# Kernel optimization log

Hardware: AMD Instinct MI355X
Metric: run time of the kernel (lower is better)

The kernel has to match this reference:

```python
import jax, jax.numpy as jnp
import numpy as np

B, T, D, K, NF = 4, 1024, 1024, 4, 4
MAXD = 256          # TemporalEncoding max_delta
NC = 32             # ConceptGraph n_concepts
LN_EPS = 1e-5


def setup_inputs() -> dict:
    key = jax.random.key(0)
    ks = jax.random.split(key, 12)
    s = 0.02  # weight init scale
    return {
        "x": jax.random.normal(ks[0], (B, T, D), jnp.float32),
        "routed_tokens": jax.random.normal(ks[1], (B, T, K, D), jnp.float32),
        "sim": jax.random.normal(ks[2], (B, T, K), jnp.float32),
        # per-function logic Linear(3D->D), LayerNorm(D), gate Linear(3D->D)
        "Wl": jax.random.normal(ks[3], (NF, 3 * D, D), jnp.float32) * s,
        "bl": jnp.zeros((NF, D), jnp.float32),
        "ln_g": jnp.ones((NF, D), jnp.float32),
        "ln_b": jnp.zeros((NF, D), jnp.float32),
        "Wg": jax.random.normal(ks[4], (NF, 3 * D, D), jnp.float32) * s,
        "bg": jnp.zeros((NF, D), jnp.float32),
        # fn_selector Linear(D -> NF)
        "Wsel": jax.random.normal(ks[5], (D, NF), jnp.float32) * s,
        "bsel": jnp.zeros((NF,), jnp.float32),
        # temporal embedding table [2*max_delta+1, D]
        "delta_table": jax.random.normal(ks[6], (2 * MAXD + 1, D), jnp.float32) * s,
        # VQ codebook (ConceptGraph.embedding buffer)
        "codebook": jax.random.normal(ks[7], (NC, D), jnp.float32),
        "topk_indices": jax.random.randint(ks[8], (B, T, K), 0, T),
    }


def reference(x, routed_tokens, sim, Wl, bl, ln_g, ln_b, Wg, bg,
              Wsel, bsel, delta_table, codebook, topk_indices):
    Bx, Tx, Dx = x.shape
    Kx = routed_tokens.shape[2]
    N = Bx * Tx

    # temporal encoding: delta = t - topk_index, clamped into table range
    t = jnp.arange(Tx)[None, :, None]
    idx = jnp.clip(t - topk_indices + MAXD, 0, 2 * MAXD)
    de = delta_table[idx].reshape(N, Kx, Dx)            # [N,K,D]

    xf = x.reshape(N, Dx)
    rf = routed_tokens.reshape(N, Kx, Dx)
    sf = sim.reshape(N, Kx)

    tok = jnp.broadcast_to(xf[:, None, :], (N, Kx, Dx))
    comb = jnp.concatenate([tok, rf, de], axis=-1)       # [N,K,3D]

    # all NF reasoning functions at once: logic MLP + GELU + LayerNorm
    h = jnp.einsum('nkc,fcd->fnkd', comb, Wl) + bl[:, None, None, :]
    h = jax.nn.gelu(h, approximate=False)
    mu = jnp.mean(h, axis=-1, keepdims=True)
    var = jnp.var(h, axis=-1, keepdims=True)
    h = (h - mu) / jnp.sqrt(var + LN_EPS)
    h = h * ln_g[:, None, None, :] + ln_b[:, None, None, :]  # [F,N,K,D]

    sw = jax.nn.softmax(sf, axis=-1)                     # [N,K]
    arg = jnp.einsum('nk,fnkd->fnd', sw, h)              # [F,N,D]

    tok_f = jnp.broadcast_to(xf[None], (Wl.shape[0], N, Dx))
    gin = jnp.concatenate([tok_f, arg, arg], axis=-1)    # [F,N,3D]
    gate = jax.nn.sigmoid(jnp.einsum('fnc,fcd->fnd', gin, Wg) + bg[:, None, :])

    fw = jax.nn.softmax(xf @ Wsel + bsel, axis=-1)       # [N,F]
    proposed = jnp.einsum('nf,fnd->nd', fw, arg)
    gsum = jnp.einsum('nf,fnd->nd', fw, gate)
    uf = proposed * gsum                                 # [N,D] updated tokens

    # ConceptGraph VQ (eval: no EMA update): pairwise dist, argmin, gather
    d2 = (jnp.sum(uf * uf, axis=1, keepdims=True)
          - 2.0 * uf @ codebook.T
          + jnp.sum(codebook * codebook, axis=1))        # [N,NC]
    enc = jnp.argmin(d2, axis=1)                         # [N]
    quant = codebook[enc]                                # [N,D]
    out = uf + jax.lax.stop_gradient(quant - uf)         # straight-through
    return out.reshape(Bx, Tx, Dx)
```

## Files before the change

### kernel.cpp

```cpp
#include <hip/hip_runtime.h>
#include <hip/hip_bf16.h>
#include <cmath>


typedef __bf16 bf16x8 __attribute__((ext_vector_type(8)));
typedef float  f32x4  __attribute__((ext_vector_type(4)));

__device__ __forceinline__ float gelu_f(float v) {
    return 0.5f * v * (1.0f + erff(v * 0.7071067811865476f));
}

__device__ __forceinline__ void split8(const float* v, bf16x8& H, bf16x8& L) {
#pragma unroll
    for (int j = 0; j < 8; ++j) {
        float x = v[j];
        __bf16 h = (__bf16)x;
        H[j] = h;
        L[j] = (__bf16)(x - (float)h);
    }
}

#define GLL16(src, dst)                                                        \
    __builtin_amdgcn_global_load_lds(                                          \
        (const __attribute__((address_space(1))) void*)(src),                  \
        (__attribute__((address_space(3))) void*)(dst), 16, 0, 0)

#define SWZ_DECODE()                                                           \
    int bx, by, bz;                                                            \
    {                                                                          \
        const int nx = gridDim.x, ny = gridDim.y;                              \
        const int nwg = nx * ny * (int)gridDim.z;                              \
        const int bid = blockIdx.x + nx * (blockIdx.y + ny * blockIdx.z);      \
        const int q = nwg >> 3;                                                \
        const int rm = (bid & 7) * q + (bid >> 3);                             \
        bx = rm % nx; by = (rm / nx) % ny; bz = rm / (nx * ny);                \
    }

__global__ __launch_bounds__(256) void precvt_img(
    const float* __restrict__ W, char* __restrict__ img,
    int krowBase, int nktLog, int sumFromKt)
{
    const int u = blockIdx.x * 256 + threadIdx.x;
    const int col = u & 127;
    const int kt  = (u >> 7) & ((1 << nktLog) - 1);
    const int ct  = (u >> (7 + nktLog)) & 7;
    const int f   = u >> (10 + nktLog);
    const int colg = ct * 128 + col;
    const float* Wf = W + (size_t)f * 3072 * 1024;
    const bool sum2 = (kt >= sumFromKt);

    float vv[32];
#pragma unroll
    for (int j = 0; j < 32; ++j) {
        int k = krowBase + kt * 32 + j;
        float v = Wf[(size_t)k * 1024 + colg];
        if (sum2) v += Wf[(size_t)(k + 1024) * 1024 + colg];
        vv[j] = v;
    }
    char* tb = img + ((((size_t)f * 8 + ct) << nktLog) + kt) * 16384;
    const int swz = (col >> 1) & 3;
#pragma unroll
    for (int g = 0; g < 4; ++g) {
        bf16x8 H, L; split8(&vv[g * 8], H, L);
        char* dst = tb + col * 64 + ((g ^ swz) << 4);
        *(bf16x8*)dst = H;
        *(bf16x8*)(dst + 8192) = L;
    }
}

#define WRITEA_SPLIT(AB)                                                       \
    {                                                                          \
        int row = tid >> 2, ag = tid & 3;                                      \
        bf16x8 H, L; split8(ra[0], H, L);                                      \
        char* d = (AB) + row * 64 + ((ag ^ ((row >> 1) & 3)) << 4);            \
        *(bf16x8*)d = H; *(bf16x8*)(d + 8192) = L;                             \
        int row2 = row + 64;                                                   \
        split8(ra[1], H, L);                                                   \
        char* d2 = (AB) + row2 * 64 + ((ag ^ ((row2 >> 1) & 3)) << 4);         \
        *(bf16x8*)d2 = H; *(bf16x8*)(d2 + 8192) = L;                           \
    }

#define LOADB_IMG(KT, BB)                                                      \
    {                                                                          \
        const char* sb = Bt + (size_t)(KT) * 16384 + boff;                     \
        char* db = (BB) + boff;                                                \
        GLL16(sb,        db);                                                  \
        GLL16(sb + 1024, db + 1024);                                           \
        GLL16(sb + 2048, db + 2048);                                           \
        GLL16(sb + 3072, db + 3072);                                           \
    }

#define MFMA32(AB, BB)                                                         \
    {                                                                          \
        bf16x8 ah[4], al[4], bh[4], bl_[4];                                    \
        _Pragma("unroll")                                                      \
        for (int mi = 0; mi < 4; ++mi) {                                       \
            const char* pa = (AB) + (wr + mi * 16 + rl) * 64 + goff;           \
            ah[mi] = *(const bf16x8*)pa;                                       \
            al[mi] = *(const bf16x8*)(pa + 8192);                              \
        }                                                                      \
        _Pragma("unroll")                                                      \
        for (int ni = 0; ni < 4; ++ni) {                                       \
            const char* pb = (BB) + (wc + ni * 16 + rl) * 64 + goff;           \
            bh[ni]  = *(const bf16x8*)pb;                                      \
            bl_[ni] = *(const bf16x8*)(pb + 8192);                             \
        }                                                                      \
        _Pragma("unroll")                                                      \
        for (int mi = 0; mi < 4; ++mi)                                         \
            _Pragma("unroll")                                                  \
            for (int ni = 0; ni < 4; ++ni) {                                   \
                acc[mi][ni] = __builtin_amdgcn_mfma_f32_16x16x32_bf16(ah[mi], bh[ni],  acc[mi][ni], 0, 0, 0); \
                acc[mi][ni] = __builtin_amdgcn_mfma_f32_16x16x32_bf16(ah[mi], bl_[ni], acc[mi][ni], 0, 0, 0); \
                acc[mi][ni] = __builtin_amdgcn_mfma_f32_16x16x32_bf16(al[mi], bh[ni],  acc[mi][ni], 0, 0, 0); \
            }                                                                  \
    }

__global__ __launch_bounds__(256, 2) void gemm_img(
    const float* __restrict__ A, int rowBase,
    const char* __restrict__ img, int fimgBase,
    float* __restrict__ C, size_t cStrideZ)
{
    __shared__ __align__(16) char lds[65536];
    const int tid = threadIdx.x, wid = tid >> 6, lane = tid & 63;
    SWZ_DECODE();
    const int bm0 = bx * 128, bn0 = by * 128;
    const int fimg = fimgBase + bz;
    const char* Bt = img + (size_t)((fimg * 8 + by) << 5) * 16384;
    float* Cp = C + (size_t)bz * cStrideZ;
    const int wr = (wid >> 1) * 64, wc = (wid & 1) * 64;
    const int g = lane >> 4, rl = lane & 15;
    const int goff = ((g ^ ((rl >> 1) & 3)) << 4);
    const int boff = wid * 4096 + lane * 16;
    char* A0 = lds;            char* A1 = lds + 16384;
    char* B0 = lds + 32768;    char* B1 = lds + 49152;

    const float* abase = A + (size_t)(rowBase + bm0 + (tid >> 2)) * 1024 + (tid & 3) * 8;
    float ra[2][8];
#define LOADA_H(KT)                                                            \
    {                                                                          \
        const float* s = abase + (KT) * 32;                                    \
        *(float4*)&ra[0][0] = ((const float4*)s)[0];                           \
        *(float4*)&ra[0][4] = ((const float4*)s)[1];                           \
        const float* s2 = s + 64 * 1024;                                       \
        *(float4*)&ra[1][0] = ((const float4*)s2)[0];                          \
        *(float4*)&ra[1][4] = ((const float4*)s2)[1];                          \
    }

    f32x4 acc[4][4];
    f32x4 zero = {0.f, 0.f, 0.f, 0.f};
#pragma unroll
    for (int i = 0; i < 4; ++i)
#pragma unroll
        for (int j = 0; j < 4; ++j) acc[i][j] = zero;

    LOADA_H(0)
    LOADB_IMG(0, B0)
    WRITEA_SPLIT(A0)
    LOADA_H(1)
    __syncthreads();
    for (int kt = 0; kt < 32; ++kt) {
        char* Ac = (kt & 1) ? A1 : A0;  char* Bc = (kt & 1) ? B1 : B0;
        char* An = (kt & 1) ? A0 : A1;  char* Bn = (kt & 1) ? B0 : B1;
        if (kt < 31) {
            LOADB_IMG(kt + 1, Bn)
            WRITEA_SPLIT(An)
            if (kt < 30) LOADA_H(kt + 2)
        }
        MFMA32(Ac, Bc)
        __syncthreads();
    }
#undef LOADA_H

    const int cg = lane & 15, rg = (lane >> 4) * 4;
#pragma unroll
    for (int mi = 0; mi < 4; ++mi)
#pragma unroll
        for (int i = 0; i < 4; ++i) {
            int row_out = bm0 + wr + mi * 16 + rg + i;
#pragma unroll
            for (int ni = 0; ni < 4; ++ni) {
                int col = bn0 + wc + ni * 16 + cg;
                Cp[(size_t)row_out * 1024 + col] = acc[mi][ni][i];
            }
        }
}

__global__ __launch_bounds__(256, 2) void gate_img(
    const float* __restrict__ x, const float* __restrict__ arg,
    const char* __restrict__ img, const float* __restrict__ fw,
    const float* __restrict__ bg, float* __restrict__ g2, int fbase)
{
    __shared__ __align__(16) char lds[65536];
    const int tid = threadIdx.x, wid = tid >> 6, lane = tid & 63;
    SWZ_DECODE();
    const int bm0 = bx * 128, bn0 = by * 128;
    const int z = bz, f = fbase + z;
    const float* argf = arg + (size_t)f * 4096 * 1024;
    const char* Bt = img + (size_t)((f * 8 + by) << 6) * 16384;
    const int wr = (wid >> 1) * 64, wc = (wid & 1) * 64;
    const int g = lane >> 4, rl = lane & 15;
    const int goff = ((g ^ ((rl >> 1) & 3)) << 4);
    const int boff = wid * 4096 + lane * 16;
    char* A0 = lds;            char* A1 = lds + 16384;
    char* B0 = lds + 32768;    char* B1 = lds + 49152;

    const int arow = bm0 + (tid >> 2);
    const int akc  = (tid & 3) * 8;
    float ra[2][8];
#define LOADA_G(KT)                                                            \
    {                                                                          \
        int k0 = (KT) * 32 + akc;                                              \
        const float* base = (k0 < 1024) ? x : (argf - 1024);                   \
        const float* s  = base + (size_t)arow * 1024 + k0;                     \
        const float* s2 = base + (size_t)(arow + 64) * 1024 + k0;              \
        *(float4*)&ra[0][0] = ((const float4*)s)[0];                           \
        *(float4*)&ra[0][4] = ((const float4*)s)[1];                           \
        *(float4*)&ra[1][0] = ((const float4*)s2)[0];                          \
        *(float4*)&ra[1][4] = ((const float4*)s2)[1];                          \
    }

    f32x4 acc[4][4];
    f32x4 zero = {0.f, 0.f, 0.f, 0.f};
#pragma unroll
    for (int i = 0; i < 4; ++i)
#pragma unroll
        for (int j = 0; j < 4; ++j) acc[i][j] = zero;

    LOADA_G(0)
    LOADB_IMG(0, B0)
    WRITEA_SPLIT(A0)
    LOADA_G(1)
    __syncthreads();
    for (int kt = 0; kt < 64; ++kt) {
        char* Ac = (kt & 1) ? A1 : A0;  char* Bc = (kt & 1) ? B1 : B0;
        char* An = (kt & 1) ? A0 : A1;  char* Bn = (kt & 1) ? B0 : B1;
        if (kt < 63) {
            LOADB_IMG(kt + 1, Bn)
            WRITEA_SPLIT(An)
            if (kt < 62) LOADA_G(kt + 2)
        }
        MFMA32(Ac, Bc)
        __syncthreads();
    }
#undef LOADA_G

    const int cg = lane & 15, rg = (lane >> 4) * 4;
    const bool accum = (fbase > 0);
#pragma unroll
    for (int mi = 0; mi < 4; ++mi)
#pragma unroll
        for (int i = 0; i < 4; ++i) {
            int row_out = bm0 + wr + mi * 16 + rg + i;
            float fwv = fw[(size_t)row_out * 4 + f];
#pragma unroll
            for (int ni = 0; ni < 4; ++ni) {
                int col = bn0 + wc + ni * 16 + cg;
                float v = acc[mi][ni][i] + bg[f * 1024 + col];
                float s = fwv / (1.0f + expf(-v));
                size_t off = ((size_t)z * 4096 + row_out) * 1024 + col;
                if (accum) g2[off] += s; else g2[off] = s;
            }
        }
}

#define STAGE_WRITE64()                                                        \
    _Pragma("unroll")                                                          \
    for (int i = 0; i < 4; ++i) {                                              \
        int u = tid + i * 256;                                                 \
        int arow = u >> 3, ag = u & 7;                                         \
        bf16x8 H, L; split8(rav[i], H, L);                                     \
        char* dst = lds + arow * 128 + ((ag ^ (arow & 7)) << 4);               \
        *(bf16x8*)dst = H; *(bf16x8*)(dst + 16384) = L;                        \
    }                                                                          \
    _Pragma("unroll")                                                          \
    for (int i = 0; i < 4; ++i) {                                              \
        int u = tid + i * 256;                                                 \
        int bcol = u & 127, bgu = u >> 7;                                      \
        bf16x8 H, L; split8(rbv[i], H, L);                                     \
        char* dst = lds + 32768 + bcol * 128 + ((bgu ^ (bcol & 7)) << 4);      \
        *(bf16x8*)dst = H; *(bf16x8*)(dst + 16384) = L;                        \
    }

#define MFMA64()                                                               \
    _Pragma("unroll")                                                          \
    for (int ks2 = 0; ks2 < 2; ++ks2) {                                        \
        bf16x8 ah[4], al[4], bh[4], bl_[4];                                    \
        _Pragma("unroll")                                                      \
        for (int mi = 0; mi < 4; ++mi) {                                       \
            const char* pa = lds + (wr + mi * 16 + rl) * 128                   \
                             + (((ks2 * 4 + g) ^ (rl & 7)) << 4);              \
            ah[mi] = *(const bf16x8*)pa;                                       \
            al[mi] = *(const bf16x8*)(pa + 16384);                             \
        }                                                                      \
        _Pragma("unroll")                                                      \
        for (int ni = 0; ni < 4; ++ni) {                                       \
            const char* pb = lds + 32768 + (wc + ni * 16 + rl) * 128           \
                             + (((ks2 * 4 + g) ^ (rl & 7)) << 4);              \
            bh[ni]  = *(const bf16x8*)pb;                                      \
            bl_[ni] = *(const bf16x8*)(pb + 16384);                            \
        }                                                                      \
        _Pragma("unroll")                                                      \
        for (int mi = 0; mi < 4; ++mi)                                         \
            _Pragma("unroll")                                                  \
            for (int ni = 0; ni < 4; ++ni) {                                   \
                acc[mi][ni] = __builtin_amdgcn_mfma_f32_16x16x32_bf16(ah[mi], bh[ni],  acc[mi][ni], 0, 0, 0); \
                acc[mi][ni] = __builtin_amdgcn_mfma_f32_16x16x32_bf16(ah[mi], bl_[ni], acc[mi][ni], 0, 0, 0); \
                acc[mi][ni] = __builtin_amdgcn_mfma_f32_16x16x32_bf16(al[mi], bh[ni],  acc[mi][ni], 0, 0, 0); \
            }                                                                  \
    }

__global__ __launch_bounds__(256, 2) void deproj_part(
    const float* __restrict__ dtab, const float* __restrict__ Wl,
    float* __restrict__ pbase)
{
    __shared__ __align__(16) char lds[65536];
    const int tid = threadIdx.x, wid = tid >> 6, lane = tid & 63;
    SWZ_DECODE();
    const int bm0 = bx * 128, bn0 = by * 128;
    const int f = bz & 3, ks = bz >> 2;
    const int akb = ks * 256;
    const float* Bf = Wl + (size_t)f * 3072 * 1024 + (size_t)(2048 + ks * 256) * 1024;
    float* Cp = pbase + (size_t)ks * 2101248 + (size_t)f * 525312;
    const int wr = (wid >> 1) * 64, wc = (wid & 1) * 64;
    const int g = lane >> 4, rl = lane & 15;

    float rav[4][8], rbv[4][8];

#define LOADA_D(KC0)                                                           \
    _Pragma("unroll")                                                          \
    for (int i = 0; i < 4; ++i) {                                              \
        int u = tid + i * 256;                                                 \
        int r = bm0 + (u >> 3); if (r > 512) r = 512;                          \
        const float* s = dtab + (size_t)r * 1024 + akb + (KC0) + (u & 7) * 8;  \
        *(float4*)&rav[i][0] = ((const float4*)s)[0];                          \
        *(float4*)&rav[i][4] = ((const float4*)s)[1];                          \
    }
#define LOADB_D(KC0)                                                           \
    _Pragma("unroll")                                                          \
    for (int i = 0; i < 4; ++i) {                                              \
        int u = tid + i * 256;                                                 \
        int bcol = bn0 + (u & 127);                                            \
        int k0 = (KC0) + (u >> 7) * 8;                                         \
        _Pragma("unroll")                                                      \
        for (int j = 0; j < 8; ++j)                                            \
            rbv[i][j] = Bf[(size_t)(k0 + j) * 1024 + bcol];                    \
    }

    f32x4 acc[4][4];
    f32x4 zero = {0.f, 0.f, 0.f, 0.f};
#pragma unroll
    for (int i = 0; i < 4; ++i)
#pragma unroll
        for (int j = 0; j < 4; ++j) acc[i][j] = zero;

    LOADA_D(0) LOADB_D(0)
    for (int kt = 0; kt < 4; ++kt) {
        STAGE_WRITE64()
        __syncthreads();
        if (kt + 1 < 4) { LOADA_D((kt + 1) * 64) LOADB_D((kt + 1) * 64) }
        MFMA64()
        __syncthreads();
    }
#undef LOADA_D
#undef LOADB_D

    const int cg = lane & 15, rg = (lane >> 4) * 4;
#pragma unroll
    for (int mi = 0; mi < 4; ++mi)
#pragma unroll
        for (int i = 0; i < 4; ++i) {
            int row_out = bm0 + wr + mi * 16 + rg + i;
            if (row_out >= 513) continue;
#pragma unroll
            for (int ni = 0; ni < 4; ++ni) {
                int col = bn0 + wc + ni * 16 + cg;
                Cp[(size_t)row_out * 1024 + col] = acc[mi][ni][i];
            }
        }
}

__global__ __launch_bounds__(256) void deproj_reduce(float* __restrict__ p)
{
    const size_t i = ((size_t)blockIdx.x * 256 + threadIdx.x) * 4;
    float4 a = *(float4*)&p[i];
    float4 b = *(const float4*)&p[i + 2101248];
    float4 c = *(const float4*)&p[i + 4202496];
    float4 d = *(const float4*)&p[i + 6303744];
    a.x = ((a.x + b.x) + c.x) + d.x;
    a.y = ((a.y + b.y) + c.y) + d.y;
    a.z = ((a.z + b.z) + c.z) + d.z;
    a.w = ((a.w + b.w) + c.w) + d.w;
    *(float4*)&p[i] = a;
}

__global__ __launch_bounds__(256) void fw_kernel(
    const float* __restrict__ x, const float* __restrict__ Wsel,
    const float* __restrict__ bsel, float* __restrict__ fw)
{
    __shared__ float sred[16];
    const int n = blockIdx.x;
    const int tid = threadIdx.x, w = tid >> 6, lane = tid & 63;

    float4 xv = *(const float4*)&x[(size_t)n * 1024 + tid * 4];
    float pf0 = 0, pf1 = 0, pf2 = 0, pf3 = 0;
    const float* wrp = &Wsel[(size_t)tid * 16];
    pf0 += xv.x * wrp[0];  pf1 += xv.x * wrp[1];  pf2 += xv.x * wrp[2];  pf3 += xv.x * wrp[3];
    pf0 += xv.y * wrp[4];  pf1 += xv.y * wrp[5];  pf2 += xv.y * wrp[6];  pf3 += xv.y * wrp[7];
    pf0 += xv.z * wrp[8];  pf1 += xv.z * wrp[9];  pf2 += xv.z * wrp[10]; pf3 += xv.z * wrp[11];
    pf0 += xv.w * wrp[12]; pf1 += xv.w * wrp[13]; pf2 += xv.w * wrp[14]; pf3 += xv.w * wrp[15];
    for (int o = 32; o; o >>= 1) {
        pf0 += __shfl_xor(pf0, o); pf1 += __shfl_xor(pf1, o);
        pf2 += __shfl_xor(pf2, o); pf3 += __shfl_xor(pf3, o);
    }
    if (lane == 0) { sred[w*4+0] = pf0; sred[w*4+1] = pf1; sred[w*4+2] = pf2; sred[w*4+3] = pf3; }
    __syncthreads();
    if (tid == 0) {
        float s0 = sred[0] + sred[4] + sred[8]  + sred[12] + bsel[0];
        float s1 = sred[1] + sred[5] + sred[9]  + sred[13] + bsel[1];
        float s2 = sred[2] + sred[6] + sred[10] + sred[14] + bsel[2];
        float s3 = sred[3] + sred[7] + sred[11] + sred[15] + bsel[3];
        float mx = fmaxf(fmaxf(s0, s1), fmaxf(s2, s3));
        float e0 = expf(s0 - mx), e1 = expf(s1 - mx), e2 = expf(s2 - mx), e3 = expf(s3 - mx);
        float inv = 1.0f / (e0 + e1 + e2 + e3);
        float4 o = { e0 * inv, e1 * inv, e2 * inv, e3 * inv };
        *(float4*)&fw[(size_t)n * 4] = o;
    }
}

__global__ __launch_bounds__(256) void ln_fuse_kernel(
    const float* __restrict__ hpre, const float* __restrict__ de_proj,
    const float* __restrict__ bl, const float* __restrict__ ln_g,
    const float* __restrict__ ln_b, const float* __restrict__ sim,
    const int* __restrict__ topk, float* arg,
    int f, int token_base, const float* xl)
{
    __shared__ float red[4 * 1024];
    const int n = token_base + blockIdx.x;
    const int k = threadIdx.x >> 6, lane = threadIdx.x & 63;
    const float* hrow = hpre + ((size_t)blockIdx.x * 4 + k) * 1024;
    const int t  = n & 1023;
    const int tk = topk[(size_t)n * 4 + k];
    int di = t - tk + 256; di = di < 0 ? 0 : (di > 512 ? 512 : di);
    const float* drow = de_proj + ((size_t)f * 513 + di) * 1024;
    const float* blr = bl + f * 1024;
    const float* gr  = ln_g + f * 1024;
    const float* br  = ln_b + f * 1024;
    const float* xr  = xl + (size_t)n * 1024;

    float4 s4 = *(const float4*)&sim[(size_t)n * 4];
    float smax = fmaxf(fmaxf(s4.x, s4.y), fmaxf(s4.z, s4.w));
    float e0 = expf(s4.x - smax), e1 = expf(s4.y - smax);
    float e2 = expf(s4.z - smax), e3 = expf(s4.w - smax);
    float swk = (k == 0 ? e0 : k == 1 ? e1 : k == 2 ? e2 : e3) / (e0 + e1 + e2 + e3);

    float gv[16];
    float ssum = 0.f;
#pragma unroll
    for (int j = 0; j < 4; ++j) {
        int d4 = lane + j * 64;
        float4 h  = *(const float4*)&hrow[d4 * 4];
        float4 dd = *(const float4*)&drow[d4 * 4];
        float4 bb = *(const float4*)&blr[d4 * 4];
        float4 xv = *(const float4*)&xr[d4 * 4];
        float a0 = gelu_f(h.x + xv.x + dd.x + bb.x);
        float a1 = gelu_f(h.y + xv.y + dd.y + bb.y);
        float a2 = gelu_f(h.z + xv.z + dd.z + bb.z);
        float a3 = gelu_f(h.w + xv.w + dd.w + bb.w);
        gv[j*4+0] = a0; gv[j*4+1] = a1; gv[j*4+2] = a2; gv[j*4+3] = a3;
        ssum += a0 + a1 + a2 + a3;
    }
    for (int o = 32; o; o >>= 1) ssum += __shfl_xor(ssum, o);
    float mu = ssum * 0.0009765625f;
    float vs = 0.f;
#pragma unroll
    for (int i = 0; i < 16; ++i) { float dm = gv[i] - mu; vs += dm * dm; }
    for (int o = 32; o; o >>= 1) vs += __shfl_xor(vs, o);
    float rstd = 1.0f / sqrtf(vs * 0.0009765625f + 1e-5f);
#pragma unroll
    for (int j = 0; j < 4; ++j) {
        int d4 = lane + j * 64;
        float4 g4 = *(const float4*)&gr[d4 * 4];
        float4 b4 = *(const float4*)&br[d4 * 4];
        float4 y;
        y.x = ((gv[j*4+0] - mu) * rstd * g4.x + b4.x) * swk;
        y.y = ((gv[j*4+1] - mu) * rstd * g4.y + b4.y) * swk;
        y.z = ((gv[j*4+2] - mu) * rstd * g4.z + b4.z) * swk;
        y.w = ((gv[j*4+3] - mu) * rstd * g4.w + b4.w) * swk;
        *(float4*)&red[k * 1024 + d4 * 4] = y;
    }
    __syncthreads();
    const int p = threadIdx.x;
    float4 r0 = *(const float4*)&red[0 * 1024 + p * 4];
    float4 r1 = *(const float4*)&red[1 * 1024 + p * 4];
    float4 r2 = *(const float4*)&red[2 * 1024 + p * 4];
    float4 r3 = *(const float4*)&red[3 * 1024 + p * 4];
    float4 o;
    o.x = r0.x + r1.x + r2.x + r3.x;
    o.y = r0.y + r1.y + r2.y + r3.y;
    o.z = r0.z + r1.z + r2.z + r3.z;
    o.w = r0.w + r1.w + r2.w + r3.w;
    *(float4*)&arg[((size_t)f * 4096 + n) * 1024 + p * 4] = o;
}

__global__ __launch_bounds__(256) void final_kernel(
    const float* __restrict__ fw, const float* __restrict__ arg,
    const float* __restrict__ g2, const float* __restrict__ cb,
    float* __restrict__ out)
{
    __shared__ float uf_s[1024];
    __shared__ float score_s[32];
    __shared__ int enc_s;
    const int n = blockIdx.x;
    const int tid = threadIdx.x, w = tid >> 6, lane = tid & 63;

    float4 fwv = *(const float4*)&fw[(size_t)n * 4];
    float fwa[4] = { fwv.x, fwv.y, fwv.z, fwv.w };

    float4 prop = {0, 0, 0, 0};
#pragma unroll
    for (int f = 0; f < 4; ++f) {
        float4 av = *(const float4*)&arg[((size_t)f * 4096 + n) * 1024 + tid * 4];
        prop.x += fwa[f] * av.x; prop.y += fwa[f] * av.y;
        prop.z += fwa[f] * av.z; prop.w += fwa[f] * av.w;
    }
    float4 ga = *(const float4*)&g2[(size_t)n * 1024 + tid * 4];
    float4 gb = *(const float4*)&g2[(size_t)(4096 + n) * 1024 + tid * 4];
    float4 uf;
    uf.x = prop.x * (ga.x + gb.x); uf.y = prop.y * (ga.y + gb.y);
    uf.z = prop.z * (ga.z + gb.z); uf.w = prop.w * (ga.w + gb.w);
    *(float4*)&uf_s[tid * 4] = uf;
    __syncthreads();

#pragma unroll
    for (int cc = 0; cc < 8; ++cc) {
        int c = w * 8 + cc;
        float p = 0.f, q = 0.f;
#pragma unroll
        for (int j = 0; j < 4; ++j) {
            int d4 = lane + j * 64;
            float4 u4 = *(const float4*)&uf_s[d4 * 4];
            float4 c4 = *(const float4*)&cb[(size_t)c * 1024 + d4 * 4];
            p += u4.x * c4.x + u4.y * c4.y + u4.z * c4.z + u4.w * c4.w;
            q += c4.x * c4.x + c4.y * c4.y + c4.z * c4.z + c4.w * c4.w;
        }
        float s = q - 2.0f * p;
        for (int o = 32; o; o >>= 1) s += __shfl_xor(s, o);
        if (lane == 0) score_s[c] = s;
    }
    __syncthreads();
    if (tid < 64) {
        float v; int idx;
        if (lane < 32) { v = score_s[lane]; idx = lane; }
        else           { v = INFINITY;      idx = 1 << 30; }
        for (int o = 16; o; o >>= 1) {
            float ov = __shfl_xor(v, o); int oi = __shfl_xor(idx, o);
            if (ov < v || (ov == v && oi < idx)) { v = ov; idx = oi; }
        }
        if (lane == 0) enc_s = idx;
    }
    __syncthreads();
    const int enc = enc_s;
    float4 o4 = *(const float4*)&cb[(size_t)enc * 1024 + tid * 4];
    *(float4*)&out[(size_t)n * 1024 + tid * 4] = o4;
}

extern "C" void kernel_launch(void* const* d_in, const int* in_sizes, int n_in,
                              void* d_out, int out_size, void* d_ws, size_t ws_size,
                              hipStream_t stream)
{
    const float* x    = (const float*)d_in[0];
    const float* rf   = (const float*)d_in[1];
    const float* sim  = (const float*)d_in[2];
    const float* Wl   = (const float*)d_in[3];
    const float* bl   = (const float*)d_in[4];
    const float* ln_g = (const float*)d_in[5];
    const float* ln_b = (const float*)d_in[6];
    const float* Wg   = (const float*)d_in[7];
    const float* bg   = (const float*)d_in[8];
    const float* Wsel = (const float*)d_in[9];
    const float* bsel = (const float*)d_in[10];
    const float* dtab = (const float*)d_in[11];
    const float* cb   = (const float*)d_in[12];
    const int*   topk = (const int*)d_in[13];
    float* out = (float*)d_out;
    dim3 blk(256);

    const size_t NEED = 142622720ull;
    if (ws_size < NEED) return;
    char* ws = (char*)d_ws;
    float* arg     = (float*)(ws + 0);
    float* de_proj = (float*)(ws + 67108864);
    float* hbuf    = (float*)(ws + 75513856);
    char*  Wl1img  = ws + 109068288;
    char*  Wl0img  = ws + 125845504;
    char*  Wgimg   = ws + 67108864;
    float* g2      = (float*)(ws + 100663296);
    float* fw      = (float*)(ws + 134217728);

    deproj_part<<<dim3(5, 8, 16), blk, 0, stream>>>(dtab, Wl, de_proj);
    deproj_reduce<<<2052, blk, 0, stream>>>(de_proj);

    precvt_img<<<512, blk, 0, stream>>>(Wl, Wl0img, 0, 5, 99);
    gemm_img<<<dim3(32, 8, 4), blk, 0, stream>>>(
        x, 0, Wl0img, 0, arg, (size_t)4096 * 1024);

    precvt_img<<<512, blk, 0, stream>>>(Wl, Wl1img, 1024, 5, 99);

    for (int f = 0; f < 4; ++f) {
        const float* xlf = arg + (size_t)f * 4096 * 1024;
        for (int ch = 0; ch < 2; ++ch) {
            gemm_img<<<dim3(64, 8, 1), blk, 0, stream>>>(
                rf, ch * 8192, Wl1img, f, hbuf, 0);
            ln_fuse_kernel<<<2048, blk, 0, stream>>>(
                hbuf, de_proj, bl, ln_g, ln_b, sim, topk, arg,
                f, ch * 2048, xlf);
        }
    }

    precvt_img<<<1024, blk, 0, stream>>>(Wg, Wgimg, 0, 6, 32);

    fw_kernel<<<4096, blk, 0, stream>>>(x, Wsel, bsel, fw);

    gate_img<<<dim3(32, 8, 2), blk, 0, stream>>>(x, arg, Wgimg, fw, bg, g2, 0);
    gate_img<<<dim3(32, 8, 2), blk, 0, stream>>>(x, arg, Wgimg, fw, bg, g2, 2);

    final_kernel<<<4096, blk, 0, stream>>>(fw, arg, g2, cb, out);
}
```

Measured before the change: 994.7 us.

## Triple-buffer B tiles with explicit vmcnt waits in GEMM pipelines

```diff
diff --git a/kernel.cpp b/kernel.cpp
--- a/kernel.cpp
+++ b/kernel.cpp
@@ -35,6 +35,13 @@
         const int rm = (bid & 7) * q + (bid >> 3);                             \
         bx = rm % nx; by = (rm / nx) % ny; bz = rm / (nx * ny);                \
     }
+
+#define WAIT_VM(N)                                                             \
+    asm volatile("s_waitcnt vmcnt(" #N ")" ::: "memory");                      \
+    __builtin_amdgcn_sched_barrier(0);
+#define WAIT_LGKM0()                                                           \
+    asm volatile("s_waitcnt lgkmcnt(0)" ::: "memory");                         \
+    __builtin_amdgcn_sched_barrier(0);
 
 __global__ __launch_bounds__(256) void precvt_img(
     const float* __restrict__ W, char* __restrict__ img,
@@ -115,12 +122,34 @@
             }                                                                  \
     }
 
+#define PIPE_LOOP(NKT, LOADA_MACRO)                                            \
+    LOADA_MACRO(0)                                                             \
+    LOADB_IMG(0, Bc0)                                                          \
+    WRITEA_SPLIT(Ac)                                                           \
+    LOADA_MACRO(1)                                                             \
+    LOADB_IMG(1, Bc1)                                                          \
+    WAIT_VM(8)                                                                 \
+    WAIT_LGKM0()                                                               \
+    __builtin_amdgcn_s_barrier();                                              \
+    for (int kt = 0; kt < (NKT); ++kt) {                                       \
+        if (kt + 1 < (NKT)) { WRITEA_SPLIT(An) }                               \
+        if (kt + 2 < (NKT)) { LOADA_MACRO(kt + 2) LOADB_IMG(kt + 2, Bc2) }     \
+        MFMA32(Ac, Bc0)                                                        \
+        if (kt + 1 < (NKT)) {                                                  \
+            if (kt + 2 < (NKT)) { WAIT_VM(8) } else { WAIT_VM(0) }             \
+            WAIT_LGKM0()                                                       \
+            __builtin_amdgcn_s_barrier();                                      \
+        }                                                                      \
+        char* bt = Bc0; Bc0 = Bc1; Bc1 = Bc2; Bc2 = bt;                        \
+        char* at = Ac; Ac = An; An = at;                                       \
+    }
+
 __global__ __launch_bounds__(256, 2) void gemm_img(
     const float* __restrict__ A, int rowBase,
     const char* __restrict__ img, int fimgBase,
     float* __restrict__ C, size_t cStrideZ)
 {
-    __shared__ __align__(16) char lds[65536];
+    __shared__ __align__(16) char lds[81920];
     const int tid = threadIdx.x, wid = tid >> 6, lane = tid & 63;
     SWZ_DECODE();
     const int bm0 = bx * 128, bn0 = by * 128;
@@ -131,8 +160,8 @@
     const int g = lane >> 4, rl = lane & 15;
     const int goff = ((g ^ ((rl >> 1) & 3)) << 4);
     const int boff = wid * 4096 + lane * 16;
-    char* A0 = lds;            char* A1 = lds + 16384;
-    char* B0 = lds + 32768;    char* B1 = lds + 49152;
+    char* Ac = lds;            char* An = lds + 16384;
+    char* Bc0 = lds + 32768;   char* Bc1 = lds + 49152;   char* Bc2 = lds + 65536;
 
     const float* abase = A + (size_t)(rowBase + bm0 + (tid >> 2)) * 1024 + (tid & 3) * 8;
     float ra[2][8];
@@ -153,22 +182,7 @@
 #pragma unroll
         for (int j = 0; j < 4; ++j) acc[i][j] = zero;
 
-    LOADA_H(0)
-    LOADB_IMG(0, B0)
-    WRITEA_SPLIT(A0)
-    LOADA_H(1)
-    __syncthreads();
-    for (int kt = 0; kt < 32; ++kt) {
-        char* Ac = (kt & 1) ? A1 : A0;  char* Bc = (kt & 1) ? B1 : B0;
-        char* An = (kt & 1) ? A0 : A1;  char* Bn = (kt & 1) ? B0 : B1;
-        if (kt < 31) {
-            LOADB_IMG(kt + 1, Bn)
-            WRITEA_SPLIT(An)
-            if (kt < 30) LOADA_H(kt + 2)
-        }
-        MFMA32(Ac, Bc)
-        __syncthreads();
-    }
+    PIPE_LOOP(32, LOADA_H)
 #undef LOADA_H
 
     const int cg = lane & 15, rg = (lane >> 4) * 4;
@@ -190,7 +204,7 @@
     const char* __restrict__ img, const float* __restrict__ fw,
     const float* __restrict__ bg, float* __restrict__ g2, int fbase)
 {
-    __shared__ __align__(16) char lds[65536];
+    __shared__ __align__(16) char lds[81920];
     const int tid = threadIdx.x, wid = tid >> 6, lane = tid & 63;
     SWZ_DECODE();
     const int bm0 = bx * 128, bn0 = by * 128;
@@ -201,8 +215,8 @@
     const int g = lane >> 4, rl = lane & 15;
     const int goff = ((g ^ ((rl >> 1) & 3)) << 4);
     const int boff = wid * 4096 + lane * 16;
-    char* A0 = lds;            char* A1 = lds + 16384;
-    char* B0 = lds + 32768;    char* B1 = lds + 49152;
+    char* Ac = lds;            char* An = lds + 16384;
+    char* Bc0 = lds + 32768;   char* Bc1 = lds + 49152;   char* Bc2 = lds + 65536;
 
     const int arow = bm0 + (tid >> 2);
     const int akc  = (tid & 3) * 8;
@@ -226,22 +240,7 @@
 #pragma unroll
         for (int j = 0; j < 4; ++j) acc[i][j] = zero;
 
-    LOADA_G(0)
-    LOADB_IMG(0, B0)
-    WRITEA_SPLIT(A0)
-    LOADA_G(1)
-    __syncthreads();
-    for (int kt = 0; kt < 64; ++kt) {
-        char* Ac = (kt & 1) ? A1 : A0;  char* Bc = (kt & 1) ? B1 : B0;
-        char* An = (kt & 1) ? A0 : A1;  char* Bn = (kt & 1) ? B0 : B1;
-        if (kt < 63) {
-            LOADB_IMG(kt + 1, Bn)
-            WRITEA_SPLIT(An)
-            if (kt < 62) LOADA_G(kt + 2)
-        }
-        MFMA32(Ac, Bc)
-        __syncthreads();
-    }
+    PIPE_LOOP(64, LOADA_G)
 #undef LOADA_G
 
     const int cg = lane & 15, rg = (lane >> 4) * 4;
```

Result: faster. 948.9 us, median of 3 (-4.6%).
